# Kernel tuning notes

Hardware: AMD Instinct MI355X
Metric: run time of the kernel (lower is better)

## Reference

```python
import jax, jax.numpy as jnp
import numpy as np
from jax import lax

GRID = 50
T_DIM = 1
Y_DIM = GRID * GRID
R_DIM = 128
Z_DIM = 64
H_DIM = 128
C_CONV = 32


def _conv(x, w, b):
    # x: [N, Cin, H, W], w: [Cout, Cin, 3, 3]
    y = lax.conv_general_dilated(x, w, (1, 1), 'SAME',
                                 dimension_numbers=('NCHW', 'OIHW', 'NCHW'))
    return y + b[None, :, None, None]


def setup_inputs() -> dict:
    key = jax.random.key(0)
    ks = jax.random.split(key, 24)
    B, NC, NT = 16, 64, 128
    s = lambda k, sh, f: (jax.random.normal(k, sh, jnp.float32) * f)
    inp = {
        'x_context': jax.random.normal(ks[0], (B, NC, T_DIM), jnp.float32),
        'y_context': jax.random.normal(ks[1], (B, NC, Y_DIM), jnp.float32),
        'x_target': jax.random.normal(ks[2], (B, NT, T_DIM), jnp.float32),
        'eps': jax.random.normal(ks[3], (B, Z_DIM), jnp.float32),
        # CNN encoder (Net)
        'w1': s(ks[4], (C_CONV, 2, 3, 3), 0.2), 'b1': jnp.zeros((C_CONV,), jnp.float32),
        'w2': s(ks[5], (C_CONV, C_CONV, 3, 3), 0.1), 'b2': jnp.zeros((C_CONV,), jnp.float32),
        'We1': s(ks[6], (C_CONV + T_DIM, H_DIM), 0.1), 'be1': jnp.zeros((H_DIM,), jnp.float32),
        'We2': s(ks[7], (H_DIM, R_DIM), 0.1), 'be2': jnp.zeros((R_DIM,), jnp.float32),
        # MuSigmaEncoder
        'Wh': s(ks[8], (R_DIM, H_DIM), 0.1), 'bh': jnp.zeros((H_DIM,), jnp.float32),
        'Wmu': s(ks[9], (H_DIM, Z_DIM), 0.1), 'bmu': jnp.zeros((Z_DIM,), jnp.float32),
        'Wsig': s(ks[10], (H_DIM, Z_DIM), 0.1), 'bsig': jnp.zeros((Z_DIM,), jnp.float32),
        # Decoder
        'Wd1': s(ks[11], (T_DIM + Z_DIM, H_DIM), 0.1), 'bd1': jnp.zeros((H_DIM,), jnp.float32),
        'Wd2': s(ks[12], (H_DIM, H_DIM), 0.1), 'bd2': jnp.zeros((H_DIM,), jnp.float32),
        'Wdmu': s(ks[13], (H_DIM, Y_DIM), 0.05), 'bdmu': jnp.zeros((Y_DIM,), jnp.float32),
        'Wdsig': s(ks[14], (H_DIM, Y_DIM), 0.05), 'bdsig': jnp.zeros((Y_DIM,), jnp.float32),
    }
    return inp


def _xy_to_mu_sigma(x, y, p):
    B, N, _ = x.shape
    x_flat = x.reshape(B * N, T_DIM)                      # [BN, 1]
    y_grid = y.reshape(B * N, 1, GRID, GRID)              # [BN,1,50,50]
    # broadcast of x value over the grid (replaces per-sample Python loop)
    x_grid = jnp.broadcast_to(x_flat[:, 0, None, None, None], (B * N, 1, GRID, GRID))
    xy_grid = jnp.concatenate([y_grid, x_grid], axis=1)   # [BN,2,50,50]
    h = jax.nn.relu(_conv(xy_grid, p['w1'], p['b1']))
    h = jax.nn.relu(_conv(h, p['w2'], p['b2']))
    pooled = h.mean(axis=(2, 3))                          # [BN, C_CONV]
    feat = jnp.concatenate([pooled, x_flat], axis=-1)     # [BN, C_CONV+1]
    r_i = jnp.dot(jax.nn.relu(jnp.dot(feat, p['We1']) + p['be1']), p['We2']) + p['be2']
    r = r_i.reshape(B, N, R_DIM).mean(axis=1)             # aggregate over points
    hr = jax.nn.relu(jnp.dot(r, p['Wh']) + p['bh'])
    mu = jnp.dot(hr, p['Wmu']) + p['bmu']
    sigma = 0.1 + 0.9 * jax.nn.sigmoid(jnp.dot(hr, p['Wsig']) + p['bsig'])
    return mu, sigma


def _decode(x_target, z, p):
    B, M, _ = x_target.shape
    z_rep = jnp.broadcast_to(z[:, None, :], (B, M, Z_DIM))
    xz = jnp.concatenate([x_target, z_rep], axis=-1)      # [B,M,1+Z]
    h = jax.nn.relu(jnp.dot(xz, p['Wd1']) + p['bd1'])
    h = jax.nn.relu(jnp.dot(h, p['Wd2']) + p['bd2'])
    y_mu = jnp.dot(h, p['Wdmu']) + p['bdmu']
    y_sigma = 0.1 + 0.9 * jax.nn.softplus(jnp.dot(h, p['Wdsig']) + p['bdsig'])
    return y_mu, y_sigma


def reference(x_context, y_context, x_target, eps,
              w1, b1, w2, b2, We1, be1, We2, be2,
              Wh, bh, Wmu, bmu, Wsig, bsig,
              Wd1, bd1, Wd2, bd2, Wdmu, bdmu, Wdsig, bdsig):
    p = dict(w1=w1, b1=b1, w2=w2, b2=b2, We1=We1, be1=be1, We2=We2, be2=be2,
             Wh=Wh, bh=bh, Wmu=Wmu, bmu=bmu, Wsig=Wsig, bsig=bsig,
             Wd1=Wd1, bd1=bd1, Wd2=Wd2, bd2=bd2, Wdmu=Wdmu, bdmu=bdmu,
             Wdsig=Wdsig, bdsig=bdsig)
    mu_c, sigma_c = _xy_to_mu_sigma(x_context, y_context, p)
    z = mu_c + sigma_c * eps                               # rsample (reparameterized)
    y_mu, y_sigma = _decode(x_target, z, p)
    return y_mu, y_sigma, mu_c, sigma_c
```

## Files before the change

### kernel.cpp

```cpp
#include <hip/hip_runtime.h>

#define GRID_N   50
#define YDIM     2500
#define BATCH    16
#define NCTX     64
#define NTGT     128
#define BN       1024
#define RDIM     128
#define ZDIM     64
#define HDIM     128
#define CCONV    32
#define NSTRIP   5
#define STRIPROWS 10

typedef __attribute__((ext_vector_type(8))) short  s8v;
typedef __attribute__((ext_vector_type(4))) float  f4v;
typedef __attribute__((ext_vector_type(4))) unsigned int u4v;

__device__ __forceinline__ unsigned short f2bf(float f) {
    unsigned int u = __float_as_uint(f);
    u += 0x7FFFu + ((u >> 16) & 1u);
    return (unsigned short)(u >> 16);
}
__device__ __forceinline__ unsigned int cvtpk(float lo, float hi) {
    unsigned int r;
    asm("v_cvt_pk_bf16_f32 %0, %1, %2" : "=v"(r) : "v"(lo), "v"(hi));
    return r;
}


#define PLB   40320
#define SMEMB 44928
#define ROWB  144


__global__ void k_pack(const float* __restrict__ w1, const float* __restrict__ b1,
                       const float* __restrict__ w2,
                       unsigned short* __restrict__ w2p, unsigned short* __restrict__ w1p,
                       float* __restrict__ tregG,
                       const float* __restrict__ Wmu, const float* __restrict__ Wsg,
                       unsigned short* __restrict__ wdp)
{
    int t = threadIdx.x;
    if (blockIdx.y == 2) {
        if (blockIdx.x != 0) return;
        int l = t & 63, qq = t >> 6;
        int cout_lo = l & 15, cb = (l >> 4) & 3;
        for (int e = qq; e < 18; e += 4) {
            int tap = e >> 1, ntt = e & 1;
            int cout = ntt * 16 + cout_lo;
            unsigned int pk[4];
#pragma unroll
            for (int g = 0; g < 4; ++g) {
                int jj = 2 * g;
                int cinL = (jj < 4) ? (cb * 4 + jj) : (16 + cb * 4 + (jj - 4));
                unsigned int lo = f2bf(w2[(cout * 32 + cinL) * 9 + tap]);
                unsigned int hi = f2bf(w2[(cout * 32 + cinL + 1) * 9 + tap]);
                pk[g] = lo | (hi << 16);
            }
            uint4 o; o.x = pk[0]; o.y = pk[1]; o.z = pk[2]; o.w = pk[3];
            *(uint4*)&w2p[((tap * 2 + ntt) * 64 + l) * 8] = o;
        }
        if (t < 128) {
            int ct = t >> 6, lane = t & 63;
            int c = ct * 16 + (lane & 15), q2 = lane >> 4;
            const signed char ktab[16] = {0,1,3,4,  6,7,2,-1,  5,-1,8,-1,  -1,-1,-1,-1};
            unsigned short v8[8];
#pragma unroll
            for (int j = 0; j < 8; ++j) {
                v8[j] = 0;
                if (j < 4) {
                    int km = ktab[q2 * 4 + j];
                    if (km >= 0) v8[j] = f2bf(w1[(c * 2 + 0) * 9 + km]);
                }
            }
            uint4 o;
            o.x = (unsigned)v8[0] | ((unsigned)v8[1] << 16);
            o.y = (unsigned)v8[2] | ((unsigned)v8[3] << 16);
            o.z = (unsigned)v8[4] | ((unsigned)v8[5] << 16);
            o.w = (unsigned)v8[6] | ((unsigned)v8[7] << 16);
            *(uint4*)&w1p[(ct * 64 + lane) * 8] = o;
        }
        for (int e = t; e < 288; e += 256) {
            int ridx = e >> 5, c = e & 31;
            int rr = ridx / 3, cc = ridx % 3;
            float sum = 0.f;
            for (int ky = 0; ky < 3; ++ky)
                for (int kx = 0; kx < 3; ++kx) {
                    bool rok = !((rr == 0 && ky == 0) || (rr == 2 && ky == 2));
                    bool cok = !((cc == 0 && kx == 0) || (cc == 2 && kx == 2));
                    if (rok && cok) sum += w1[(c * 2 + 1) * 9 + ky * 3 + kx];
                }
            tregG[e] = sum;
        }
        return;
    }
    int nt = blockIdx.x;
    int which = blockIdx.y;
    const float* W = which ? Wsg : Wmu;
    unsigned short* outp = wdp + (size_t)which * (157 * 4 * 64 * 8);
    int l = t & 63, ks = t >> 6;
    int n = nt * 16 + (l & 15);
    int kbase = ks * 32 + ((l >> 4) & 3) * 8;
    unsigned int pk[4];
#pragma unroll
    for (int g = 0; g < 4; ++g) {
        float f0 = (n < 2500) ? W[(kbase + 2 * g) * 2500 + n] : 0.f;
        float f1 = (n < 2500) ? W[(kbase + 2 * g + 1) * 2500 + n] : 0.f;
        pk[g] = (unsigned int)f2bf(f0) | ((unsigned int)f2bf(f1) << 16);
    }
    uint4 o; o.x = pk[0]; o.y = pk[1]; o.z = pk[2]; o.w = pk[3];
    *(uint4*)&outp[((nt * 4 + ks) * 64 + l) * 8] = o;
}

__global__ __launch_bounds__(512, 6) void k_conv(
    const float* __restrict__ xc, const float* __restrict__ yc,
    const unsigned short* __restrict__ w1p, const unsigned short* __restrict__ w2p,
    const float* __restrict__ b1, const float* __restrict__ b2,
    const float* __restrict__ tregG, float* __restrict__ part)
{
    __shared__ __align__(16) char smem[SMEMB];
    unsigned short* pl = (unsigned short*)(smem + PLB);
    float* redbuf = (float*)smem;

    const int t = threadIdx.x, lane = t & 63, w = t >> 6;
    const int l15 = lane & 15, q = lane >> 4;
    const int par = lane & 1;
    const int blk = blockIdx.x, s = blk / NSTRIP, strip = blk - s * NSTRIP;
    const int r0 = strip * STRIPROWS;

    const float xv = xc[s];
    const float b2v0 = b2[l15], b2v1 = b2[16 + l15];
    const float4 bv0 = *(const float4*)&b1[q * 4];
    const float4 bv1 = *(const float4*)&b1[16 + q * 4];
    const f4v bC0 = {bv0.x, bv0.y, bv0.z, bv0.w};
    const f4v bC1 = {bv1.x, bv1.y, bv1.z, bv1.w};
    const f4v cb0 = {b2v0, b2v0, b2v0, b2v0};
    const f4v cb1 = {b2v1, b2v1, b2v1, b2v1};

    if (t == 0) pl[0] = 0;
    for (int e = t; e < 736; e += 512) {
        unsigned ry = ((unsigned)(e * 1261)) >> 16;
        int ycol = e - (int)ry * 52;
        int gy = r0 - 2 + (int)ry, gc = ycol - 1;
        unsigned short yb = 0;
        if (((unsigned)gy < 50u) && ((unsigned)gc < 50u))
            yb = f2bf(yc[s * YDIM + gy * 50 + gc]);
        pl[1 + e] = yb;
        if (e < 734) pl[738 + e] = yb;
    }

    s8v w1f[2];
#pragma unroll
    for (int ct = 0; ct < 2; ++ct)
        w1f[ct] = *(const s8v*)&w1p[(ct * 64 + lane) * 8];

    int Ba = (q == 0) ? -1 : (q == 1) ? 103 : (q == 2) ? 53 : -1;
    int Bb = (q == 0) ? 51 : (q == 1) ? 1 : (q == 2) ? 105 : -1;
    auto mkoff = [&](int B) {
        int pr = (B + 1 + par) & 1;
        return PLB + (pr ? 2 * (738 + B) : 2 * (1 + B)) + 2 * l15;
    };
    const int go0 = mkoff(Ba), go1 = mkoff(Bb);
    const int wo = (l15 >> 1) * ROWB + (l15 & 1) * 64 + q * 16;

    __syncthreads();

    auto do_tile = [&](int mt) -> uint4 {
        int mo = mt * 32;
        unsigned g0 = *(const unsigned*)(smem + go0 + mo);
        unsigned g1 = *(const unsigned*)(smem + go1 + mo);
        u4v gg = {g0, g1, 0u, 0u};
        s8v af = __builtin_bit_cast(s8v, gg);
        f4v c0 = __builtin_amdgcn_mfma_f32_16x16x32_bf16(w1f[0], af, bC0, 0, 0, 0);
        f4v c1 = __builtin_amdgcn_mfma_f32_16x16x32_bf16(w1f[1], af, bC1, 0, 0, 0);
        int m = mt * 16 + l15;
        unsigned mr = ((unsigned)(m * 1261)) >> 16;
        int mc = m - (int)mr * 52;
        int gy = r0 - 1 + (int)mr;
        int gc = mc - 1;
        bool valid = ((unsigned)gc < 50u) && ((unsigned)gy < 50u);
        int rr = (gy == 0) ? 0 : ((gy == 49) ? 2 : 1);
        int cc = (gc == 0) ? 0 : ((gc == 49) ? 2 : 1);
        int ridx = rr * 3 + cc;
        float4 tg0 = *(const float4*)&tregG[ridx * 32 + q * 4];
        float4 tg1 = *(const float4*)&tregG[ridx * 32 + 16 + q * 4];
        c0[0] = fmaf(xv, tg0.x, c0[0]);
        c0[1] = fmaf(xv, tg0.y, c0[1]);
        c0[2] = fmaf(xv, tg0.z, c0[2]);
        c0[3] = fmaf(xv, tg0.w, c0[3]);
        c1[0] = fmaf(xv, tg1.x, c1[0]);
        c1[1] = fmaf(xv, tg1.y, c1[1]);
        c1[2] = fmaf(xv, tg1.z, c1[2]);
        c1[3] = fmaf(xv, tg1.w, c1[3]);
        unsigned p0 = cvtpk(fmaxf(c0[0], 0.f), fmaxf(c0[1], 0.f));
        unsigned p1 = cvtpk(fmaxf(c0[2], 0.f), fmaxf(c0[3], 0.f));
        unsigned p2 = cvtpk(fmaxf(c1[0], 0.f), fmaxf(c1[1], 0.f));
        unsigned p3 = cvtpk(fmaxf(c1[2], 0.f), fmaxf(c1[3], 0.f));
        if (!valid) { p0 = 0u; p1 = 0u; p2 = 0u; p3 = 0u; }
        return make_uint4(p0, p1, p2, p3);
    };
    auto wr_tile = [&](int mt, uint4 v) {
        *(uint4*)(smem + wo + mt * 1152) = v;
    };

#pragma unroll 5
    for (int it = 0; it < 5; ++it) {
        int mt = w + it * 8;
        if (mt <= 34) {
            uint4 v = do_tile(mt);
            wr_tile(mt, v);
        }
    }
    {
        bool hold = (w < 4);
        uint4 hA = make_uint4(0u, 0u, 0u, 0u);
        int mt0 = 35 + w;
        if (hold) hA = do_tile(mt0);
        __syncthreads();
        if (hold) wr_tile(mt0, hA);
    }
    __syncthreads();

    f4v acc[4][2];
#pragma unroll
    for (int i = 0; i < 4; ++i) { acc[i][0] = cb0; acc[i][1] = cb1; }
    int bE[4], bO[4];
#pragma unroll
    for (int tt = 0; tt < 4; ++tt) {
        int m2 = (w * 4 + tt) * 16 + l15;
        unsigned orr = ((unsigned)(m2 * 1311)) >> 16;
        int pu = (m2 + 2 * (int)orr) >> 1;
        pu = (pu > 258) ? 258 : pu;
        bE[tt] = pu * ROWB + (par << 6) + (q << 4);
        bO[tt] = bE[tt] + (par ? 80 : 64);
    }
    __builtin_amdgcn_s_setprio(1);
#pragma unroll
    for (int tp = 0; tp < 9; ++tp) {
        const int ky = tp / 3, kx = tp % 3;
        const int off = 3744 * ky + (kx == 2 ? ROWB : 0);
        s8v b0 = *(const s8v*)&w2p[((tp * 2 + 0) * 64 + lane) * 8];
        s8v b1f = *(const s8v*)&w2p[((tp * 2 + 1) * 64 + lane) * 8];
#pragma unroll
        for (int tt = 0; tt < 4; ++tt) {
            s8v a = *(const s8v*)(smem + (kx == 1 ? bO[tt] : bE[tt]) + off);
            acc[tt][0] = __builtin_amdgcn_mfma_f32_16x16x32_bf16(a, b0, acc[tt][0], 0, 0, 0);
            acc[tt][1] = __builtin_amdgcn_mfma_f32_16x16x32_bf16(a, b1f, acc[tt][1], 0, 0, 0);
        }
    }
    __builtin_amdgcn_s_setprio(0);

    float ps0 = 0.f, ps1 = 0.f;
#pragma unroll
    for (int tt = 0; tt < 4; ++tt) {
        int tile = w * 4 + tt;
        if (tile != 31) {
#pragma unroll
            for (int r = 0; r < 4; ++r) {
                ps0 += fmaxf(acc[tt][0][r], 0.f);
                ps1 += fmaxf(acc[tt][1][r], 0.f);
            }
        } else {
            int mbase = tile * 16 + q * 4;
#pragma unroll
            for (int r = 0; r < 4; ++r) {
                if (mbase + r < 500) {
                    ps0 += fmaxf(acc[tt][0][r], 0.f);
                    ps1 += fmaxf(acc[tt][1][r], 0.f);
                }
            }
        }
    }
    ps0 += __shfl_xor(ps0, 16); ps0 += __shfl_xor(ps0, 32);
    ps1 += __shfl_xor(ps1, 16); ps1 += __shfl_xor(ps1, 32);
    __syncthreads();
    if (lane < 16) {
        redbuf[w * 32 + l15] = ps0;
        redbuf[w * 32 + 16 + l15] = ps1;
    }
    __syncthreads();
    if (t < 32) {
        float v = 0.f;
#pragma unroll
        for (int k = 0; k < 8; ++k) v += redbuf[k * 32 + t];
        part[(s * NSTRIP + strip) * 32 + t] = v;
    }
}

__global__ void k_enc(const float* __restrict__ part, const float* __restrict__ xc,
                      const float* __restrict__ We1, const float* __restrict__ be1,
                      const float* __restrict__ We2, const float* __restrict__ be2,
                      float* __restrict__ r_i)
{
    __shared__ float feat[33];
    __shared__ float h[128];
    int s = blockIdx.x, j = threadIdx.x;
    if (j < 32) {
        float v = 0.f;
#pragma unroll
        for (int st = 0; st < NSTRIP; ++st) v += part[(s * NSTRIP + st) * 32 + j];
        feat[j] = v * (1.f / 2500.f);
    }
    if (j == 0) feat[32] = xc[s];
    __syncthreads();
    float a = be1[j];
#pragma unroll 4
    for (int k = 0; k < 33; ++k) a = fmaf(feat[k], We1[k * 128 + j], a);
    h[j] = fmaxf(a, 0.f);
    __syncthreads();
    float r = be2[j];
#pragma unroll 8
    for (int k = 0; k < 128; ++k) r = fmaf(h[k], We2[k * 128 + j], r);
    r_i[s * 128 + j] = r;
}

__global__ void k_ms(const float* __restrict__ r_i,
                     const float* __restrict__ Wh, const float* __restrict__ bh,
                     const float* __restrict__ Wmu, const float* __restrict__ bmu,
                     const float* __restrict__ Wsig, const float* __restrict__ bsig,
                     const float* __restrict__ eps, float* __restrict__ out,
                     float* __restrict__ zbuf)
{
    __shared__ float r[128], hr[128], tmp[2][128];
    int b = blockIdx.x, t = threadIdx.x;
    int j = t & 127, g = t >> 7;
    float acc = 0.f;
#pragma unroll 4
    for (int i = g; i < NCTX; i += 2) acc += r_i[(b * NCTX + i) * 128 + j];
    tmp[g][j] = acc;
    __syncthreads();
    if (g == 0) r[j] = (tmp[0][j] + tmp[1][j]) * (1.f / 64.f);
    __syncthreads();
    float a = (g == 0) ? bh[j] : 0.f;
#pragma unroll 8
    for (int k = g * 64; k < g * 64 + 64; ++k) a = fmaf(r[k], Wh[k * 128 + j], a);
    tmp[g][j] = a;
    __syncthreads();
    if (g == 0) hr[j] = fmaxf(tmp[0][j] + tmp[1][j], 0.f);
    __syncthreads();
    if (j < 64) {
        float m = (g == 0) ? bmu[j] : 0.f, sg = (g == 0) ? bsig[j] : 0.f;
#pragma unroll 8
        for (int k = g * 64; k < g * 64 + 64; ++k) {
            m  = fmaf(hr[k], Wmu[k * 64 + j], m);
            sg = fmaf(hr[k], Wsig[k * 64 + j], sg);
        }
        tmp[g][j] = m; tmp[g][64 + j] = sg;
    }
    __syncthreads();
    if (t < 64) {
        float m  = tmp[0][t] + tmp[1][t];
        float sg = tmp[0][64 + t] + tmp[1][64 + t];
        float sig = 0.1f + 0.9f / (1.f + expf(-sg));
        out[10240000 + b * 64 + t] = m;
        out[10241024 + b * 64 + t] = sig;
        zbuf[b * 64 + t] = m + sig * eps[b * 64 + t];
    }
}

__global__ __launch_bounds__(256) void k_dec1(
    const float* __restrict__ xt, const float* __restrict__ zbuf,
    const float* __restrict__ Wd1, const float* __restrict__ bd1,
    const float* __restrict__ Wd2, const float* __restrict__ bd2,
    unsigned short* __restrict__ h2d)
{
    __shared__ float zsh[64];
    __shared__ float vsh[2][128];
    __shared__ float h1sh[4][128];
    int t = threadIdx.x;
    int j = t & 127, g = t >> 7;
    int r0 = blockIdx.x * 4;
    int b = r0 >> 7;
    if (t < 64) zsh[t] = zbuf[b * 64 + t];
    __syncthreads();
    float v = (g == 0) ? bd1[j] : 0.f;
#pragma unroll 8
    for (int k = g * 32; k < g * 32 + 32; ++k)
        v = fmaf(zsh[k], Wd1[(1 + k) * 128 + j], v);
    vsh[g][j] = v;
    __syncthreads();
    float vv = vsh[0][j] + vsh[1][j];
    float w0 = Wd1[j];
    int ra = r0 + g * 2;
    float x0 = xt[ra], x1 = xt[ra + 1];
    h1sh[g * 2][j]     = fmaxf(fmaf(x0, w0, vv), 0.f);
    h1sh[g * 2 + 1][j] = fmaxf(fmaf(x1, w0, vv), 0.f);
    __syncthreads();
    float bd2j = bd2[j];
    float a0 = bd2j, a1 = bd2j;
#pragma unroll 8
    for (int k = 0; k < 128; ++k) {
        float wv = Wd2[k * 128 + j];
        a0 = fmaf(h1sh[g * 2][k], wv, a0);
        a1 = fmaf(h1sh[g * 2 + 1][k], wv, a1);
    }
    h2d[(size_t)ra * 128 + j]       = f2bf(fmaxf(a0, 0.f));
    h2d[(size_t)(ra + 1) * 128 + j] = f2bf(fmaxf(a1, 0.f));
}

__global__ __launch_bounds__(256) void k_gemm(
    const unsigned short* __restrict__ h2d, const unsigned short* __restrict__ wdp,
    const float* __restrict__ bdmu, const float* __restrict__ bdsg,
    float* __restrict__ out)
{
    __shared__ __align__(16) unsigned short Al[64 * 128];
    int t = threadIdx.x, lane = t & 63, w = t >> 6;
    int m0 = blockIdx.x * 64;
#pragma unroll
    for (int i = 0; i < 4; ++i) {
        int g = t + i * 256;
        int row = g >> 4, bk = g & 15;
        uint4 v = *(const uint4*)&h2d[(size_t)(m0 + row) * 128 + bk * 8];
        *(uint4*)&Al[row * 128 + ((bk ^ (row & 7)) << 3)] = v;
    }
    __syncthreads();
    int nt = blockIdx.y * 4 + w;
    if (nt < 157) {
        int lcol = lane & 15, lq = lane >> 4;
        int col = nt * 16 + lcol;
#pragma unroll
        for (int which = 0; which < 2; ++which) {
            const unsigned short* wp = wdp + (size_t)which * (157 * 4 * 64 * 8);
            s8v bfr[4];
#pragma unroll
            for (int ks = 0; ks < 4; ++ks)
                bfr[ks] = *(const s8v*)&wp[((nt * 4 + ks) * 64 + lane) * 8];
            f4v acc[4];
            {
                f4v zf = {0.f, 0.f, 0.f, 0.f};
#pragma unroll
                for (int mt = 0; mt < 4; ++mt) acc[mt] = zf;
            }
#pragma unroll
            for (int mt = 0; mt < 4; ++mt) {
                int mrow = mt * 16 + lcol;
#pragma unroll
                for (int ks = 0; ks < 4; ++ks) {
                    int bk = ks * 4 + lq;
                    s8v a = *(const s8v*)&Al[mrow * 128 + ((bk ^ (mrow & 7)) << 3)];
                    acc[mt] = __builtin_amdgcn_mfma_f32_16x16x32_bf16(a, bfr[ks], acc[mt], 0, 0, 0);
                }
            }
            if (col < 2500) {
                const float* bp = which ? bdsg : bdmu;
                float bv = bp[col];
                size_t zoff = (size_t)which * 5120000;
#pragma unroll
                for (int mt = 0; mt < 4; ++mt)
#pragma unroll
                    for (int r = 0; r < 4; ++r) {
                        int row = m0 + mt * 16 + lq * 4 + r;
                        float vv = acc[mt][r] + bv;
                        if (which) {
                            float sp = fmaxf(vv, 0.f) + log1pf(expf(-fabsf(vv)));
                            vv = 0.1f + 0.9f * sp;
                        }
                        out[zoff + (size_t)row * 2500 + col] = vv;
                    }
            }
        }
    }
}

extern "C" void kernel_launch(void* const* d_in, const int* in_sizes, int n_in,
                              void* d_out, int out_size, void* d_ws, size_t ws_size,
                              hipStream_t stream)
{
    const float* xc   = (const float*)d_in[0];
    const float* yc   = (const float*)d_in[1];
    const float* xt   = (const float*)d_in[2];
    const float* eps  = (const float*)d_in[3];
    const float* w1   = (const float*)d_in[4];
    const float* b1   = (const float*)d_in[5];
    const float* w2   = (const float*)d_in[6];
    const float* b2   = (const float*)d_in[7];
    const float* We1  = (const float*)d_in[8];
    const float* be1  = (const float*)d_in[9];
    const float* We2  = (const float*)d_in[10];
    const float* be2  = (const float*)d_in[11];
    const float* Wh   = (const float*)d_in[12];
    const float* bh   = (const float*)d_in[13];
    const float* Wmu  = (const float*)d_in[14];
    const float* bmu  = (const float*)d_in[15];
    const float* Wsig = (const float*)d_in[16];
    const float* bsig = (const float*)d_in[17];
    const float* Wd1  = (const float*)d_in[18];
    const float* bd1  = (const float*)d_in[19];
    const float* Wd2  = (const float*)d_in[20];
    const float* bd2  = (const float*)d_in[21];
    const float* Wdmu = (const float*)d_in[22];
    const float* bdmu = (const float*)d_in[23];
    const float* Wdsg = (const float*)d_in[24];
    const float* bdsg = (const float*)d_in[25];

    float* out = (float*)d_out;
    char* wsb  = (char*)d_ws;
    unsigned short* w2p = (unsigned short*)(wsb + 0);
    unsigned short* wdp = (unsigned short*)(wsb + 18432);
    float* part = (float*)(wsb + 1304576);
    float* r_i  = (float*)(wsb + 1959936);
    float* zbuf = (float*)(wsb + 2484224);
    unsigned short* h2d = (unsigned short*)(wsb + 2488320);
    unsigned short* w1p = (unsigned short*)(wsb + 3012608);
    float* treg = (float*)(wsb + 3014656);

    hipLaunchKernelGGL(k_pack, dim3(157, 3), dim3(256), 0, stream,
                       w1, b1, w2, w2p, w1p, treg, Wdmu, Wdsg, wdp);
    hipLaunchKernelGGL(k_conv, dim3(BN * NSTRIP), dim3(512), 0, stream,
                       xc, yc, w1p, w2p, b1, b2, treg, part);
    hipLaunchKernelGGL(k_enc, dim3(BN), dim3(128), 0, stream,
                       part, xc, We1, be1, We2, be2, r_i);
    hipLaunchKernelGGL(k_ms, dim3(BATCH), dim3(256), 0, stream,
                       r_i, Wh, bh, Wmu, bmu, Wsig, bsig, eps, out, zbuf);
    hipLaunchKernelGGL(k_dec1, dim3(512), dim3(256), 0, stream,
                       xt, zbuf, Wd1, bd1, Wd2, bd2, h2d);
    hipLaunchKernelGGL(k_gemm, dim3(32, 40), dim3(256), 0, stream,
                       h2d, wdp, bdmu, bdsg, out);
}
```

Before: 117.9 us.

## Move decoder weight packing into conv grid and split-K encoder/decoder MLPs

The large bf16 packing of the decoder output weights now runs as extra tail blocks of the conv kernel instead of in the pack kernel, so it overlaps with conv work, and the pack kernel shrinks to one block. The encoder MLP and the first decoder kernel now split the 128-deep reduction across two thread groups and combine the halves through shared memory, which doubles parallelism per block. The extra blocks in the conv launch use 512-thread blocks for light work and add a branch. The split reductions cost an extra sync and shared-memory traffic.

Result: slower. 127.0 us (+7.7%).

```diff
diff --git a/kernel.cpp b/kernel.cpp
--- a/kernel.cpp
+++ b/kernel.cpp
@@ -12,6 +12,7 @@
 #define CCONV    32
 #define NSTRIP   5
 #define STRIPROWS 10
+#define NCONVBLK (BN * NSTRIP)
 
 typedef __attribute__((ext_vector_type(8))) short  s8v;
 typedef __attribute__((ext_vector_type(4))) float  f4v;
@@ -34,91 +35,93 @@
 #define ROWB  144
 
 
-__global__ void k_pack(const float* __restrict__ w1, const float* __restrict__ b1,
-                       const float* __restrict__ w2,
-                       unsigned short* __restrict__ w2p, unsigned short* __restrict__ w1p,
-                       float* __restrict__ tregG,
-                       const float* __restrict__ Wmu, const float* __restrict__ Wsg,
-                       unsigned short* __restrict__ wdp)
+__global__ void k_pack_small(const float* __restrict__ w1, const float* __restrict__ b1,
+                             const float* __restrict__ w2,
+                             unsigned short* __restrict__ w2p, unsigned short* __restrict__ w1p,
+                             float* __restrict__ tregG)
 {
     int t = threadIdx.x;
-    if (blockIdx.y == 2) {
-        if (blockIdx.x != 0) return;
-        int l = t & 63, qq = t >> 6;
-        int cout_lo = l & 15, cb = (l >> 4) & 3;
-        for (int e = qq; e < 18; e += 4) {
-            int tap = e >> 1, ntt = e & 1;
-            int cout = ntt * 16 + cout_lo;
-            unsigned int pk[4];
-#pragma unroll
-            for (int g = 0; g < 4; ++g) {
-                int jj = 2 * g;
-                int cinL = (jj < 4) ? (cb * 4 + jj) : (16 + cb * 4 + (jj - 4));
-                unsigned int lo = f2bf(w2[(cout * 32 + cinL) * 9 + tap]);
-                unsigned int hi = f2bf(w2[(cout * 32 + cinL + 1) * 9 + tap]);
-                pk[g] = lo | (hi << 16);
-            }
-            uint4 o; o.x = pk[0]; o.y = pk[1]; o.z = pk[2]; o.w = pk[3];
-            *(uint4*)&w2p[((tap * 2 + ntt) * 64 + l) * 8] = o;
-        }
-        if (t < 128) {
-            int ct = t >> 6, lane = t & 63;
-            int c = ct * 16 + (lane & 15), q2 = lane >> 4;
-            const signed char ktab[16] = {0,1,3,4,  6,7,2,-1,  5,-1,8,-1,  -1,-1,-1,-1};
-            unsigned short v8[8];
-#pragma unroll
-            for (int j = 0; j < 8; ++j) {
-                v8[j] = 0;
-                if (j < 4) {
-                    int km = ktab[q2 * 4 + j];
-                    if (km >= 0) v8[j] = f2bf(w1[(c * 2 + 0) * 9 + km]);
-                }
-            }
-            uint4 o;
-            o.x = (unsigned)v8[0] | ((unsigned)v8[1] << 16);
-            o.y = (unsigned)v8[2] | ((unsigned)v8[3] << 16);
-            o.z = (unsigned)v8[4] | ((unsigned)v8[5] << 16);
-            o.w = (unsigned)v8[6] | ((unsigned)v8[7] << 16);
-            *(uint4*)&w1p[(ct * 64 + lane) * 8] = o;
-        }
-        for (int e = t; e < 288; e += 256) {
-            int ridx = e >> 5, c = e & 31;
-            int rr = ridx / 3, cc = ridx % 3;
-            float sum = 0.f;
-            for (int ky = 0; ky < 3; ++ky)
-                for (int kx = 0; kx < 3; ++kx) {
-                    bool rok = !((rr == 0 && ky == 0) || (rr == 2 && ky == 2));
-                    bool cok = !((cc == 0 && kx == 0) || (cc == 2 && kx == 2));
-                    if (rok && cok) sum += w1[(c * 2 + 1) * 9 + ky * 3 + kx];
-                }
-            tregG[e] = sum;
-        }
-        return;
-    }
-    int nt = blockIdx.x;
-    int which = blockIdx.y;
-    const float* W = which ? Wsg : Wmu;
-    unsigned short* outp = wdp + (size_t)which * (157 * 4 * 64 * 8);
-    int l = t & 63, ks = t >> 6;
-    int n = nt * 16 + (l & 15);
-    int kbase = ks * 32 + ((l >> 4) & 3) * 8;
-    unsigned int pk[4];
-#pragma unroll
-    for (int g = 0; g < 4; ++g) {
-        float f0 = (n < 2500) ? W[(kbase + 2 * g) * 2500 + n] : 0.f;
-        float f1 = (n < 2500) ? W[(kbase + 2 * g + 1) * 2500 + n] : 0.f;
-        pk[g] = (unsigned int)f2bf(f0) | ((unsigned int)f2bf(f1) << 16);
-    }
-    uint4 o; o.x = pk[0]; o.y = pk[1]; o.z = pk[2]; o.w = pk[3];
-    *(uint4*)&outp[((nt * 4 + ks) * 64 + l) * 8] = o;
+    int l = t & 63, qq = t >> 6;
+    int cout_lo = l & 15, cb = (l >> 4) & 3;
+    for (int e = qq; e < 18; e += 4) {
+        int tap = e >> 1, ntt = e & 1;
+        int cout = ntt * 16 + cout_lo;
+        unsigned int pk[4];
+#pragma unroll
+        for (int g = 0; g < 4; ++g) {
+            int jj = 2 * g;
+            int cinL = (jj < 4) ? (cb * 4 + jj) : (16 + cb * 4 + (jj - 4));
+            unsigned int lo = f2bf(w2[(cout * 32 + cinL) * 9 + tap]);
+            unsigned int hi = f2bf(w2[(cout * 32 + cinL + 1) * 9 + tap]);
+            pk[g] = lo | (hi << 16);
+        }
+        uint4 o; o.x = pk[0]; o.y = pk[1]; o.z = pk[2]; o.w = pk[3];
+        *(uint4*)&w2p[((tap * 2 + ntt) * 64 + l) * 8] = o;
+    }
+    if (t < 128) {
+        int ct = t >> 6, lane = t & 63;
+        int c = ct * 16 + (lane & 15), q2 = lane >> 4;
+        const signed char ktab[16] = {0,1,3,4,  6,7,2,-1,  5,-1,8,-1,  -1,-1,-1,-1};
+        unsigned short v8[8];
+#pragma unroll
+        for (int j = 0; j < 8; ++j) {
+            v8[j] = 0;
+            if (j < 4) {
+                int km = ktab[q2 * 4 + j];
+                if (km >= 0) v8[j] = f2bf(w1[(c * 2 + 0) * 9 + km]);
+            }
+        }
+        uint4 o;
+        o.x = (unsigned)v8[0] | ((unsigned)v8[1] << 16);
+        o.y = (unsigned)v8[2] | ((unsigned)v8[3] << 16);
+        o.z = (unsigned)v8[4] | ((unsigned)v8[5] << 16);
+        o.w = (unsigned)v8[6] | ((unsigned)v8[7] << 16);
+        *(uint4*)&w1p[(ct * 64 + lane) * 8] = o;
+    }
+    for (int e = t; e < 288; e += 256) {
+        int ridx = e >> 5, c = e & 31;
+        int rr = ridx / 3, cc = ridx % 3;
+        float sum = 0.f;
+        for (int ky = 0; ky < 3; ++ky)
+            for (int kx = 0; kx < 3; ++kx) {
+                bool rok = !((rr == 0 && ky == 0) || (rr == 2 && ky == 2));
+                bool cok = !((cc == 0 && kx == 0) || (cc == 2 && kx == 2));
+                if (rok && cok) sum += w1[(c * 2 + 1) * 9 + ky * 3 + kx];
+            }
+        tregG[e] = sum;
+    }
 }
 
 __global__ __launch_bounds__(512, 6) void k_conv(
     const float* __restrict__ xc, const float* __restrict__ yc,
     const unsigned short* __restrict__ w1p, const unsigned short* __restrict__ w2p,
     const float* __restrict__ b1, const float* __restrict__ b2,
-    const float* __restrict__ tregG, float* __restrict__ part)
-{
+    const float* __restrict__ tregG, float* __restrict__ part,
+    const float* __restrict__ Wdmu, const float* __restrict__ Wdsg,
+    unsigned short* __restrict__ wdp)
+{
+    const int blk = blockIdx.x;
+    if (blk >= NCONVBLK) {
+        int nt = blk - NCONVBLK;
+        int t2 = threadIdx.x & 255;
+        int which = threadIdx.x >> 8;
+        const float* W = which ? Wdsg : Wdmu;
+        unsigned short* outp = wdp + (size_t)which * (157 * 4 * 64 * 8);
+        int l = t2 & 63, ks = t2 >> 6;
+        int n = nt * 16 + (l & 15);
+        int kbase = ks * 32 + ((l >> 4) & 3) * 8;
+        unsigned int pk[4];
+#pragma unroll
+        for (int g = 0; g < 4; ++g) {
+            float f0 = (n < 2500) ? W[(kbase + 2 * g) * 2500 + n] : 0.f;
+            float f1 = (n < 2500) ? W[(kbase + 2 * g + 1) * 2500 + n] : 0.f;
+            pk[g] = (unsigned int)f2bf(f0) | ((unsigned int)f2bf(f1) << 16);
+        }
+        uint4 o; o.x = pk[0]; o.y = pk[1]; o.z = pk[2]; o.w = pk[3];
+        *(uint4*)&outp[((nt * 4 + ks) * 64 + l) * 8] = o;
+        return;
+    }
+
     __shared__ __align__(16) char smem[SMEMB];
     unsigned short* pl = (unsigned short*)(smem + PLB);
     float* redbuf = (float*)smem;
@@ -126,7 +129,7 @@
     const int t = threadIdx.x, lane = t & 63, w = t >> 6;
     const int l15 = lane & 15, q = lane >> 4;
     const int par = lane & 1;
-    const int blk = blockIdx.x, s = blk / NSTRIP, strip = blk - s * NSTRIP;
+    const int s = blk / NSTRIP, strip = blk - s * NSTRIP;
     const int r0 = strip * STRIPROWS;
 
     const float xv = xc[s];
@@ -288,31 +291,38 @@
     }
 }
 
-__global__ void k_enc(const float* __restrict__ part, const float* __restrict__ xc,
-                      const float* __restrict__ We1, const float* __restrict__ be1,
-                      const float* __restrict__ We2, const float* __restrict__ be2,
-                      float* __restrict__ r_i)
+__global__ __launch_bounds__(256) void k_enc(
+    const float* __restrict__ part, const float* __restrict__ xc,
+    const float* __restrict__ We1, const float* __restrict__ be1,
+    const float* __restrict__ We2, const float* __restrict__ be2,
+    float* __restrict__ r_i)
 {
     __shared__ float feat[33];
     __shared__ float h[128];
-    int s = blockIdx.x, j = threadIdx.x;
-    if (j < 32) {
+    __shared__ float acc2[2][128];
+    int s = blockIdx.x, t = threadIdx.x;
+    int j = t & 127, g = t >> 7;
+    if (t < 32) {
         float v = 0.f;
 #pragma unroll
-        for (int st = 0; st < NSTRIP; ++st) v += part[(s * NSTRIP + st) * 32 + j];
-        feat[j] = v * (1.f / 2500.f);
-    }
-    if (j == 0) feat[32] = xc[s];
-    __syncthreads();
-    float a = be1[j];
+        for (int st = 0; st < NSTRIP; ++st) v += part[(s * NSTRIP + st) * 32 + t];
+        feat[t] = v * (1.f / 2500.f);
+    }
+    if (t == 0) feat[32] = xc[s];
+    __syncthreads();
+    if (g == 0) {
+        float a = be1[j];
 #pragma unroll 4
-    for (int k = 0; k < 33; ++k) a = fmaf(feat[k], We1[k * 128 + j], a);
-    h[j] = fmaxf(a, 0.f);
-    __syncthreads();
-    float r = be2[j];
+        for (int k = 0; k < 33; ++k) a = fmaf(feat[k], We1[k * 128 + j], a);
+        h[j] = fmaxf(a, 0.f);
+    }
+    __syncthreads();
+    float r = (g == 0) ? be2[j] : 0.f;
 #pragma unroll 8
-    for (int k = 0; k < 128; ++k) r = fmaf(h[k], We2[k * 128 + j], r);
-    r_i[s * 128 + j] = r;
+    for (int k = g * 64; k < g * 64 + 64; ++k) r = fmaf(h[k], We2[k * 128 + j], r);
+    acc2[g][j] = r;
+    __syncthreads();
+    if (g == 0) r_i[s * 128 + j] = acc2[0][j] + acc2[1][j];
 }
 
 __global__ void k_ms(const float* __restrict__ r_i,
@@ -368,6 +378,7 @@
     __shared__ float zsh[64];
     __shared__ float vsh[2][128];
     __shared__ float h1sh[4][128];
+    __shared__ float acc2[2][4][128];
     int t = threadIdx.x;
     int j = t & 127, g = t >> 7;
     int r0 = blockIdx.x * 4;
@@ -382,21 +393,33 @@
     __syncthreads();
     float vv = vsh[0][j] + vsh[1][j];
     float w0 = Wd1[j];
-    int ra = r0 + g * 2;
-    float x0 = xt[ra], x1 = xt[ra + 1];
-    h1sh[g * 2][j]     = fmaxf(fmaf(x0, w0, vv), 0.f);
-    h1sh[g * 2 + 1][j] = fmaxf(fmaf(x1, w0, vv), 0.f);
-    __syncthreads();
-    float bd2j = bd2[j];
-    float a0 = bd2j, a1 = bd2j;
+    {
+        int ra = r0 + g * 2;
+        float x0 = xt[ra], x1 = xt[ra + 1];
+        h1sh[g * 2][j]     = fmaxf(fmaf(x0, w0, vv), 0.f);
+        h1sh[g * 2 + 1][j] = fmaxf(fmaf(x1, w0, vv), 0.f);
+    }
+    __syncthreads();
+    float bd2j = (g == 0) ? bd2[j] : 0.f;
+    float a0 = bd2j, a1 = bd2j, a2 = bd2j, a3 = bd2j;
 #pragma unroll 8
-    for (int k = 0; k < 128; ++k) {
+    for (int k = g * 64; k < g * 64 + 64; ++k) {
         float wv = Wd2[k * 128 + j];
-        a0 = fmaf(h1sh[g * 2][k], wv, a0);
-        a1 = fmaf(h1sh[g * 2 + 1][k], wv, a1);
-    }
-    h2d[(size_t)ra * 128 + j]       = f2bf(fmaxf(a0, 0.f));
-    h2d[(size_t)(ra + 1) * 128 + j] = f2bf(fmaxf(a1, 0.f));
+        a0 = fmaf(h1sh[0][k], wv, a0);
+        a1 = fmaf(h1sh[1][k], wv, a1);
+        a2 = fmaf(h1sh[2][k], wv, a2);
+        a3 = fmaf(h1sh[3][k], wv, a3);
+    }
+    acc2[g][0][j] = a0; acc2[g][1][j] = a1;
+    acc2[g][2][j] = a2; acc2[g][3][j] = a3;
+    __syncthreads();
+    {
+        int u0 = g * 2;
+#pragma unroll
+        for (int u = u0; u < u0 + 2; ++u)
+            h2d[(size_t)(r0 + u) * 128 + j] =
+                f2bf(fmaxf(acc2[0][u][j] + acc2[1][u][j], 0.f));
+    }
 }
 
 __global__ __launch_bounds__(256) void k_gemm(
@@ -505,11 +528,11 @@
     unsigned short* w1p = (unsigned short*)(wsb + 3012608);
     float* treg = (float*)(wsb + 3014656);
 
-    hipLaunchKernelGGL(k_pack, dim3(157, 3), dim3(256), 0, stream,
-                       w1, b1, w2, w2p, w1p, treg, Wdmu, Wdsg, wdp);
-    hipLaunchKernelGGL(k_conv, dim3(BN * NSTRIP), dim3(512), 0, stream,
-                       xc, yc, w1p, w2p, b1, b2, treg, part);
-    hipLaunchKernelGGL(k_enc, dim3(BN), dim3(128), 0, stream,
+    hipLaunchKernelGGL(k_pack_small, dim3(1), dim3(256), 0, stream,
+                       w1, b1, w2, w2p, w1p, treg);
+    hipLaunchKernelGGL(k_conv, dim3(NCONVBLK + 157), dim3(512), 0, stream,
+                       xc, yc, w1p, w2p, b1, b2, treg, part, Wdmu, Wdsg, wdp);
+    hipLaunchKernelGGL(k_enc, dim3(BN), dim3(256), 0, stream,
                        part, xc, We1, be1, We2, be2, r_i);
     hipLaunchKernelGGL(k_ms, dim3(BATCH), dim3(256), 0, stream,
                        r_i, Wh, bh, Wmu, bmu, Wsig, bsig, eps, out, zbuf);
```
